# Kernel tuning notes

Measured on AMD Instinct MI355X. Metric: run time of the kernel, lower is better.

## Reference

```python
import jax, jax.numpy as jnp
import numpy as np

N, NFEAT, NHID, NCLASS, ATT = 4096, 512, 128, 16, 64


def _glorot(key, shape):
    lim = 1.0 / np.sqrt(shape[0])
    return jax.random.uniform(key, shape, jnp.float32, -lim, lim)


def setup_inputs() -> dict:
    key = jax.random.key(0)
    ks = jax.random.split(key, 26)
    inp = {
        "A0": jax.random.uniform(ks[0], (N, N), jnp.float32),
        "A1": jax.random.uniform(ks[1], (N, N), jnp.float32),
        "A2": jax.random.uniform(ks[2], (N, N), jnp.float32),
        "x": jax.random.normal(ks[3], (N, NFEAT), jnp.float32),
        # attention-over-adjacency projections: Linear(N, ATT)
        "Wa1": _glorot(ks[4], (N, ATT)), "ba1": jnp.zeros((ATT,), jnp.float32),
        "Wa2": _glorot(ks[5], (N, ATT)), "ba2": jnp.zeros((ATT,), jnp.float32),
        "Wa3": _glorot(ks[6], (N, ATT)), "ba3": jnp.zeros((ATT,), jnp.float32),
        # agg: Linear(3*ATT, 3)
        "Wagg": _glorot(ks[7], (3 * ATT, 3)), "bagg": jnp.zeros((3,), jnp.float32),
        # gcn1: nfeat -> nhid
        "W1": _glorot(ks[8], (NFEAT, NHID)), "b1": jnp.zeros((NHID,), jnp.float32),
        # Q/K/V: nhid -> nhid
        "Wq": _glorot(ks[9], (NHID, NHID)), "bq": jnp.zeros((NHID,), jnp.float32),
        "Wk": _glorot(ks[10], (NHID, NHID)), "bk": jnp.zeros((NHID,), jnp.float32),
        "Wv": _glorot(ks[11], (NHID, NHID)), "bv": jnp.zeros((NHID,), jnp.float32),
        # gcn2: nhid -> nclass
        "W2": _glorot(ks[12], (NHID, NCLASS)), "b2": jnp.zeros((NCLASS,), jnp.float32),
    }
    return inp


def _gcn_norm(a):
    # symmetric degree normalization D^-1/2 A D^-1/2 (zero-safe)
    d = a.sum(axis=1)
    dinv = jnp.where(d > 0, jax.lax.rsqrt(jnp.maximum(d, 1e-12)), 0.0)
    return dinv[:, None] * a * dinv[None, :]


def reference(A0, A1, A2, x, Wa1, ba1, Wa2, ba2, Wa3, ba3, Wagg, bagg,
              W1, b1, Wq, bq, Wk, bk, Wv, bv, W2, b2):
    # per-adjacency attention logits over rows -> mixing weights per node
    z1 = A0 @ Wa1 + ba1                      # [N, ATT]
    z2 = A1 @ Wa2 + ba2
    z3 = A2 @ Wa3 + ba3
    z4 = jnp.concatenate([z1, z2, z3], axis=1) @ Wagg + bagg   # [N, 3]
    nz = jax.nn.softmax(z4, axis=1)
    # torch broadcasting: nz[:, k] (shape [N]) scales COLUMNS of [N,N]
    adj = (A0 * nz[:, 0][None, :] + A1 * nz[:, 1][None, :]
           + A2 * nz[:, 2][None, :])                           # [N, N]
    # gcn1 + relu
    h = jax.nn.relu(adj @ (x @ W1) + b1)                       # [N, NHID]
    Qh = h @ Wq + bq
    Kh = h @ Wk + bk
    Vh = h @ Wv + bv
    # adjacency-masked QK^T, row softmax, degree norm, mix with V
    A_tilde = adj * (Qh @ Kh.T)                                # [N, N]
    attention = jax.nn.softmax(A_tilde, axis=1)
    X_tilde = jax.nn.relu(_gcn_norm(attention) @ Vh)           # [N, NHID]
    # gcn2
    z = adj @ (X_tilde @ W2) + b2                              # [N, NCLASS]
    return jax.nn.softmax(z, axis=1), nz
```

## Files before the change

### kernel.cpp

```cpp
#include <hip/hip_runtime.h>
#include <math.h>

#define N 4096
#define NF 512
#define NH 128
#define NC 16
#define CSPLIT 8

typedef unsigned short u16;
typedef __attribute__((ext_vector_type(4))) unsigned short u16x4;
typedef __attribute__((ext_vector_type(8))) short bf16x8;
typedef __attribute__((ext_vector_type(4))) float f32x4;

__device__ __forceinline__ u16 hi16(float v) {
  return (u16)(__float_as_uint(v) >> 16);
}
__device__ __forceinline__ float hif(float v) {
  return __uint_as_float(__float_as_uint(v) & 0xffff0000u);
}

__global__ void k_wc(const float* __restrict__ Wa1, const float* __restrict__ Wa2,
                     const float* __restrict__ Wa3, const float* __restrict__ Wagg,
                     const float* __restrict__ ba1, const float* __restrict__ ba2,
                     const float* __restrict__ ba3, const float* __restrict__ bagg,
                     float* __restrict__ Wc2, float* __restrict__ bz) {
  int idx = blockIdx.x * 256 + threadIdx.x;
  if (idx < 3 * N) {
    int k = idx >> 12;
    int j = idx & (N - 1);
    const float* Wa = (k == 0) ? Wa1 : (k == 1) ? Wa2 : Wa3;
    float a0 = 0.f, a1 = 0.f, a2 = 0.f;
    for (int t = 0; t < 64; ++t) {
      float w = Wa[j * 64 + t];
      const float* wg = Wagg + (k * 64 + t) * 3;
      a0 += w * wg[0]; a1 += w * wg[1]; a2 += w * wg[2];
    }
    float4 o = {a0, a1, a2, 0.f};
    *(float4*)&Wc2[(k * N + j) * 4] = o;
  }
  if (blockIdx.x == 0 && threadIdx.x < 3) {
    int c = threadIdx.x;
    float acc = bagg[c];
    for (int t = 0; t < 64; ++t) {
      acc += ba1[t] * Wagg[t * 3 + c]
           + ba2[t] * Wagg[(64 + t) * 3 + c]
           + ba3[t] * Wagg[(128 + t) * 3 + c];
    }
    bz[c] = acc;
  }
}

__global__ __launch_bounds__(256) void k_z4p(const float* __restrict__ A,
                                             const float* __restrict__ Wck,
                                             float* __restrict__ zpk) {
  __shared__ float red[4][3][4];
  int r0 = blockIdx.x * 4;
  int tid = threadIdx.x;
  int lane = tid & 63, wv = tid >> 6;
  float acc[4][3];
#pragma unroll
  for (int r = 0; r < 4; ++r) { acc[r][0] = 0.f; acc[r][1] = 0.f; acc[r][2] = 0.f; }
#pragma unroll
  for (int s = 0; s < 4; ++s) {
    int j4 = s * 1024 + tid * 4;
    const float4 w0 = *(const float4*)&Wck[(j4 + 0) * 4];
    const float4 w1 = *(const float4*)&Wck[(j4 + 1) * 4];
    const float4 w2 = *(const float4*)&Wck[(j4 + 2) * 4];
    const float4 w3 = *(const float4*)&Wck[(j4 + 3) * 4];
#pragma unroll
    for (int r = 0; r < 4; ++r) {
      const float4 a = *(const float4*)&A[(size_t)(r0 + r) * N + j4];
      acc[r][0] += a.x * w0.x + a.y * w1.x + a.z * w2.x + a.w * w3.x;
      acc[r][1] += a.x * w0.y + a.y * w1.y + a.z * w2.y + a.w * w3.y;
      acc[r][2] += a.x * w0.z + a.y * w1.z + a.z * w2.z + a.w * w3.z;
    }
  }
#pragma unroll
  for (int r = 0; r < 4; ++r) {
#pragma unroll
    for (int c = 0; c < 3; ++c) {
      float v = acc[r][c];
      v += __shfl_xor(v, 1);
      v += __shfl_xor(v, 2);
      v += __shfl_xor(v, 4);
      v += __shfl_xor(v, 8);
      v += __shfl_xor(v, 16);
      v += __shfl_xor(v, 32);
      if (lane == 0) red[r][c][wv] = v;
    }
  }
  __syncthreads();
  if (tid < 12) {
    int r = tid / 3; int c = tid - 3 * r;
    zpk[(r0 + r) * 12 + c] =
        red[r][c][0] + red[r][c][1] + red[r][c][2] + red[r][c][3];
  }
}

__global__ void k_nz(const float* __restrict__ zp, const float* __restrict__ bz,
                     float* __restrict__ nz) {
  int row = blockIdx.x * 256 + threadIdx.x;
  const float* p = zp + row * 12;
  float z0 = p[0] + p[3] + p[6] + bz[0];
  float z1 = p[1] + p[4] + p[7] + bz[1];
  float z2 = p[2] + p[5] + p[8] + bz[2];
  float m = fmaxf(z0, fmaxf(z1, z2));
  float e0 = __expf(z0 - m), e1 = __expf(z1 - m), e2 = __expf(z2 - m);
  float s = e0 + e1 + e2;
  float* o = nz + row * 3;
  o[0] = e0 / s; o[1] = e1 / s; o[2] = e2 / s;
}

__global__ void k_adj(const float* __restrict__ A0, const float* __restrict__ A1,
                      const float* __restrict__ A2, const float* __restrict__ nz,
                      float* __restrict__ adj) {
  int idx = blockIdx.x * 256 + threadIdx.x;
  int i = idx >> 10;
  int j4 = (idx & 1023) << 2;
  int base = i * N + j4;
  const float4 a0 = *(const float4*)&A0[base];
  const float4 a1 = *(const float4*)&A1[base];
  const float4 a2 = *(const float4*)&A2[base];
  const float4 n0 = *(const float4*)&nz[j4 * 3];
  const float4 n1 = *(const float4*)&nz[j4 * 3 + 4];
  const float4 n2 = *(const float4*)&nz[j4 * 3 + 8];
  float4 o;
  o.x = a0.x * n0.x + a1.x * n0.y + a2.x * n0.z;
  o.y = a0.y * n0.w + a1.y * n1.x + a2.y * n1.y;
  o.z = a0.z * n1.z + a1.z * n1.w + a2.z * n2.x;
  o.w = a0.w * n2.y + a1.w * n2.z + a2.w * n2.w;
  *(float4*)&adj[base] = o;
}

__global__ void k_wsplit(const float* __restrict__ Wq, const float* __restrict__ Wk,
                         const float* __restrict__ Wv, const float* __restrict__ W1,
                         u16* __restrict__ WThi, u16* __restrict__ WTlo,
                         u16* __restrict__ W1Thi, u16* __restrict__ W1Tlo) {
  int idx = blockIdx.x * 256 + threadIdx.x;
  if (idx < 49152) {
    int gm = idx >> 14;
    int rem = idx & 16383;
    int col = rem >> 7, k = rem & 127;
    const float* W = (gm == 0) ? Wq : (gm == 1) ? Wk : Wv;
    float v = W[k * NH + col];
    WThi[idx] = hi16(v);
    WTlo[idx] = hi16(v - hif(v));
  } else {
    int rem = idx - 49152;
    int col = rem >> 9, k = rem & 511;
    float v = W1[k * NH + col];
    W1Thi[rem] = hi16(v);
    W1Tlo[rem] = hi16(v - hif(v));
  }
}

__global__ __launch_bounds__(256) void k_xw1m(
    const float* __restrict__ x,
    const u16* __restrict__ W1Thi, const u16* __restrict__ W1Tlo,
    u16* __restrict__ xw1Thi, u16* __restrict__ xw1Tlo) {
  __shared__ u16 Ah[64][128];
  __shared__ u16 Al[64][128];
  __shared__ u16 Vst[2][128 * 24];
  int i0 = blockIdx.x * 16;
  int tid = threadIdx.x;
  int w = tid >> 6, l = tid & 63, g = l >> 4, l15 = l & 15;
  {
    int r = tid >> 4, cb = (tid & 15) * 4;
#pragma unroll
    for (int q = 0; q < 4; ++q) {
      int c = cb + q;
      const float4 a0 = *(const float4*)&x[(size_t)(i0 + r) * NF + c * 8];
      const float4 a1 = *(const float4*)&x[(size_t)(i0 + r) * NF + c * 8 + 4];
      bf16x8 hi8, lo8;
      const float* p0 = (const float*)&a0;
      const float* p1 = (const float*)&a1;
#pragma unroll
      for (int e = 0; e < 4; ++e) {
        float v0 = p0[e], v1 = p1[e];
        hi8[e] = (short)hi16(v0); hi8[4 + e] = (short)hi16(v1);
        lo8[e] = (short)hi16(v0 - hif(v0));
        lo8[4 + e] = (short)hi16(v1 - hif(v1));
      }
      *(bf16x8*)&Ah[c][r * 8] = hi8;
      *(bf16x8*)&Al[c][r * 8] = lo8;
    }
  }
  __syncthreads();
  f32x4 acc[2];
  acc[0] = (f32x4){0.f, 0.f, 0.f, 0.f};
  acc[1] = (f32x4){0.f, 0.f, 0.f, 0.f};
#pragma unroll 4
  for (int kb = 0; kb < 16; ++kb) {
    const bf16x8 ah = *(const bf16x8*)&Ah[kb * 4 + g][l15 * 8];
    const bf16x8 al = *(const bf16x8*)&Al[kb * 4 + g][l15 * 8];
#pragma unroll
    for (int cti = 0; cti < 2; ++cti) {
      int col = (2 * w + cti) * 16 + l15;
      const bf16x8 bh = *(const bf16x8*)&W1Thi[col * NF + kb * 32 + 8 * g];
      const bf16x8 bl = *(const bf16x8*)&W1Tlo[col * NF + kb * 32 + 8 * g];
      acc[cti] = __builtin_amdgcn_mfma_f32_16x16x32_bf16(ah, bh, acc[cti], 0, 0, 0);
      acc[cti] = __builtin_amdgcn_mfma_f32_16x16x32_bf16(ah, bl, acc[cti], 0, 0, 0);
      acc[cti] = __builtin_amdgcn_mfma_f32_16x16x32_bf16(al, bh, acc[cti], 0, 0, 0);
    }
  }
#pragma unroll
  for (int cti = 0; cti < 2; ++cti) {
    int col = (2 * w + cti) * 16 + l15;
#pragma unroll
    for (int i = 0; i < 4; ++i) {
      float v = acc[cti][i];
      Vst[0][col * 24 + 4 * g + i] = hi16(v);
      Vst[1][col * 24 + 4 * g + i] = hi16(v - hif(v));
    }
  }
  __syncthreads();
  {
    int d = tid >> 1, half = tid & 1;
    bf16x8 vh = *(const bf16x8*)&Vst[0][d * 24 + half * 8];
    bf16x8 vl = *(const bf16x8*)&Vst[1][d * 24 + half * 8];
    *(bf16x8*)&xw1Thi[(size_t)d * N + i0 + half * 8] = vh;
    *(bf16x8*)&xw1Tlo[(size_t)d * N + i0 + half * 8] = vl;
  }
}

__device__ __forceinline__ void glds16(const void* g, void* l) {
  __builtin_amdgcn_global_load_lds(
      (const __attribute__((address_space(1))) void*)g,
      (__attribute__((address_space(3))) void*)l, 16, 0, 0);
}

__global__ __launch_bounds__(512) void k_h(const float* __restrict__ adj,
                                           const u16* __restrict__ xw1Thi,
                                           const u16* __restrict__ xw1Tlo,
                                           float* __restrict__ hp0,
                                           float* __restrict__ hp1,
                                           float* __restrict__ hp2,
                                           float* __restrict__ hp3) {
  __shared__ u16 Ah[8][512];
  __shared__ u16 Al[8][512];
  __shared__ u16 Bh[8][1024];
  __shared__ u16 Bl[8][1024];
  int i0 = blockIdx.x * 64;
  int kbase = blockIdx.y * 1024;
  float* hp = (blockIdx.y == 0) ? hp0 : (blockIdx.y == 1) ? hp1
            : (blockIdx.y == 2) ? hp2 : hp3;
  int tid = threadIdx.x;
  int w = tid >> 6, l = tid & 63, g = l >> 4, l15 = l & 15;
  int rt = w & 3, cg = w >> 2;
  int srow = tid >> 3, sseg = tid & 7;

  f32x4 acc[4];
#pragma unroll
  for (int nt = 0; nt < 4; ++nt) acc[nt] = (f32x4){0.f, 0.f, 0.f, 0.f};

  for (int t = 0; t < 16; ++t) {
    int k0 = kbase + t * 64;
    const float4 av0 = *(const float4*)&adj[(size_t)(i0 + srow) * N + k0 + sseg * 8];
    const float4 av1 = *(const float4*)&adj[(size_t)(i0 + srow) * N + k0 + sseg * 8 + 4];
    asm volatile("s_waitcnt lgkmcnt(0)" ::: "memory");
    __builtin_amdgcn_s_barrier();
#pragma unroll
    for (int q = 0; q < 4; ++q) {
      int idx = w * 4 + q;
      int buf = idx >> 4, kk = (idx >> 1) & 7, hf = idx & 1;
      const u16* src = buf ? xw1Tlo : xw1Thi;
      u16* dst = buf ? &Bl[kk][hf * 512] : &Bh[kk][hf * 512];
      glds16(&src[(size_t)(hf * 64 + l) * N + k0 + kk * 8], dst);
    }
    asm volatile("s_waitcnt vmcnt(4)" ::: "memory");
    {
      bf16x8 hi8, lo8;
      const float* a0p = (const float*)&av0;
      const float* a1p = (const float*)&av1;
#pragma unroll
      for (int e = 0; e < 4; ++e) {
        float v0 = a0p[e], v1 = a1p[e];
        hi8[e] = (short)hi16(v0);     hi8[4 + e] = (short)hi16(v1);
        lo8[e] = (short)hi16(v0 - hif(v0));
        lo8[4 + e] = (short)hi16(v1 - hif(v1));
      }
      *(bf16x8*)&Ah[sseg][srow * 8] = hi8;
      *(bf16x8*)&Al[sseg][srow * 8] = lo8;
    }
    asm volatile("s_waitcnt vmcnt(0) lgkmcnt(0)" ::: "memory");
    __builtin_amdgcn_s_barrier();

#pragma unroll
    for (int kb = 0; kb < 2; ++kb) {
      const bf16x8 ah = *(const bf16x8*)&Ah[kb * 4 + g][(rt * 16 + l15) * 8];
      const bf16x8 al = *(const bf16x8*)&Al[kb * 4 + g][(rt * 16 + l15) * 8];
#pragma unroll
      for (int nt = 0; nt < 4; ++nt) {
        int col = cg * 64 + nt * 16 + l15;
        const bf16x8 bh = *(const bf16x8*)&Bh[kb * 4 + g][col * 8];
        const bf16x8 bl = *(const bf16x8*)&Bl[kb * 4 + g][col * 8];
        acc[nt] = __builtin_amdgcn_mfma_f32_16x16x32_bf16(ah, bh, acc[nt], 0, 0, 0);
        acc[nt] = __builtin_amdgcn_mfma_f32_16x16x32_bf16(ah, bl, acc[nt], 0, 0, 0);
        acc[nt] = __builtin_amdgcn_mfma_f32_16x16x32_bf16(al, bh, acc[nt], 0, 0, 0);
      }
    }
  }
#pragma unroll
  for (int nt = 0; nt < 4; ++nt)
#pragma unroll
    for (int i = 0; i < 4; ++i)
      hp[(size_t)(i0 + rt * 16 + 4 * g + i) * NH + cg * 64 + nt * 16 + l15] =
          acc[nt][i];
}

__global__ void k_hsum(const float* __restrict__ hp0, const float* __restrict__ hp1,
                       const float* __restrict__ hp2, const float* __restrict__ hp3,
                       const float* __restrict__ b1,
                       u16* __restrict__ Hhi, u16* __restrict__ Hlo) {
  int idx = blockIdx.x * 256 + threadIdx.x;
  int gi = idx * 4;
  const float4 v0 = *(const float4*)&hp0[gi];
  const float4 v1 = *(const float4*)&hp1[gi];
  const float4 v2 = *(const float4*)&hp2[gi];
  const float4 v3 = *(const float4*)&hp3[gi];
  const float4 bv = *(const float4*)&b1[gi & (NH - 1)];
  float h[4];
  h[0] = fmaxf(v0.x + v1.x + v2.x + v3.x + bv.x, 0.f);
  h[1] = fmaxf(v0.y + v1.y + v2.y + v3.y + bv.y, 0.f);
  h[2] = fmaxf(v0.z + v1.z + v2.z + v3.z + bv.z, 0.f);
  h[3] = fmaxf(v0.w + v1.w + v2.w + v3.w + bv.w, 0.f);
  u16x4 hi, lo;
#pragma unroll
  for (int e = 0; e < 4; ++e) {
    hi[e] = hi16(h[e]);
    lo[e] = hi16(h[e] - hif(h[e]));
  }
  *(u16x4*)&Hhi[gi] = hi;
  *(u16x4*)&Hlo[gi] = lo;
}

__global__ __launch_bounds__(256) void k_qkv2(
    const u16* __restrict__ Hhi, const u16* __restrict__ Hlo,
    const u16* __restrict__ WThi, const u16* __restrict__ WTlo,
    const float* __restrict__ bq, const float* __restrict__ bk,
    const float* __restrict__ bv,
    u16* __restrict__ Qhi, u16* __restrict__ Qlo,
    u16* __restrict__ Khi, u16* __restrict__ Klo,
    u16* __restrict__ VThi, u16* __restrict__ VTlo) {
  __shared__ u16 Vst[2][128 * 24];
  int i0 = blockIdx.x * 16;
  int tid = threadIdx.x;
  int w = tid >> 6, l = tid & 63, g = l >> 4, l15 = l & 15;
  bf16x8 ah[4], al[4];
#pragma unroll
  for (int kb = 0; kb < 4; ++kb) {
    ah[kb] = *(const bf16x8*)&Hhi[(i0 + l15) * NH + kb * 32 + 8 * g];
    al[kb] = *(const bf16x8*)&Hlo[(i0 + l15) * NH + kb * 32 + 8 * g];
  }
#pragma unroll
  for (int gm = 0; gm < 3; ++gm) {
    const u16* wth = WThi + gm * 16384;
    const u16* wtl = WTlo + gm * 16384;
    const float* bb = (gm == 0) ? bq : (gm == 1) ? bk : bv;
#pragma unroll
    for (int cti = 0; cti < 2; ++cti) {
      int ct = 2 * w + cti;
      int col = ct * 16 + l15;
      f32x4 acc = (f32x4){0.f, 0.f, 0.f, 0.f};
#pragma unroll
      for (int kb = 0; kb < 4; ++kb) {
        const bf16x8 bh = *(const bf16x8*)&wth[col * NH + kb * 32 + 8 * g];
        const bf16x8 bl = *(const bf16x8*)&wtl[col * NH + kb * 32 + 8 * g];
        acc = __builtin_amdgcn_mfma_f32_16x16x32_bf16(ah[kb], bh, acc, 0, 0, 0);
        acc = __builtin_amdgcn_mfma_f32_16x16x32_bf16(ah[kb], bl, acc, 0, 0, 0);
        acc = __builtin_amdgcn_mfma_f32_16x16x32_bf16(al[kb], bh, acc, 0, 0, 0);
      }
      float bias = bb[col];
#pragma unroll
      for (int i = 0; i < 4; ++i) {
        float v = acc[i] + bias;
        u16 vh = hi16(v), vl = hi16(v - hif(v));
        int row = i0 + 4 * g + i;
        if (gm == 0) {
          Qhi[row * NH + col] = vh; Qlo[row * NH + col] = vl;
        } else if (gm == 1) {
          Khi[row * NH + col] = vh; Klo[row * NH + col] = vl;
        } else {
          Vst[0][col * 24 + 4 * g + i] = vh;
          Vst[1][col * 24 + 4 * g + i] = vl;
        }
      }
    }
  }
  __syncthreads();
  {
    int d = tid >> 1, half = tid & 1;
    bf16x8 vh = *(const bf16x8*)&Vst[0][d * 24 + half * 8];
    bf16x8 vl = *(const bf16x8*)&Vst[1][d * 24 + half * 8];
    *(bf16x8*)&VThi[(size_t)d * N + i0 + half * 8] = vh;
    *(bf16x8*)&VTlo[(size_t)d * N + i0 + half * 8] = vl;
  }
}

__global__ __launch_bounds__(512) void k_attn(
    const u16* __restrict__ Qhi, const u16* __restrict__ Qlo,
    const u16* __restrict__ Khi, const u16* __restrict__ Klo,
    const u16* __restrict__ VThi, const u16* __restrict__ VTlo,
    const float* __restrict__ adj,
    float* __restrict__ xp0, float* __restrict__ xp1, float* __restrict__ xp2,
    float* __restrict__ xp3, float* __restrict__ xp4, float* __restrict__ xp5,
    float* __restrict__ xp6, float* __restrict__ xp7,
    float* __restrict__ ml) {
  __shared__ u16 Ks[2][16][512];
  __shared__ u16 Vs[2][8][1024];
  __shared__ u16 Ps[2][8][1024];
  int i0 = blockIdx.x * 128;
  int cid = blockIdx.y;
  int tid = threadIdx.x;
  int w = tid >> 6, l = tid & 63, g = l >> 4, l15 = l & 15;
  int ty = tid >> 4, tx16 = tid & 15;
  float* xp = (cid < 4) ? ((cid < 2) ? (cid == 0 ? xp0 : xp1) : (cid == 2 ? xp2 : xp3))
                        : ((cid < 6) ? (cid == 4 ? xp4 : xp5) : (cid == 6 ? xp6 : xp7));

  bf16x8 qh[4], ql[4];
  {
    const u16* qbh = &Qhi[(i0 + 16 * w + l15) * NH];
    const u16* qbl = &Qlo[(i0 + 16 * w + l15) * NH];
#pragma unroll
    for (int kb = 0; kb < 4; ++kb) {
      qh[kb] = *(const bf16x8*)&qbh[kb * 32 + 8 * g];
      ql[kb] = *(const bf16x8*)&qbl[kb * 32 + 8 * g];
    }
  }

  float m[4], li[4];
  f32x4 Xa[8];
#pragma unroll
  for (int i = 0; i < 4; ++i) { m[i] = -3.0e38f; li[i] = 0.f; }
#pragma unroll
  for (int nt = 0; nt < 8; ++nt) Xa[nt] = (f32x4){0.f, 0.f, 0.f, 0.f};

  for (int jt = 0; jt < 8; ++jt) {
    int j0g = cid * (N / CSPLIT) + jt * 64;
    float adjm[4][4];
#pragma unroll
    for (int i = 0; i < 4; ++i)
#pragma unroll
      for (int ct = 0; ct < 4; ++ct)
        adjm[i][ct] = adj[(i0 + 4 * ty + i) * N + j0g + ct * 16 + tx16];
    asm volatile("s_waitcnt lgkmcnt(0)" ::: "memory");
    __builtin_amdgcn_s_barrier();
#pragma unroll
    for (int q = 0; q < 4; ++q) {
      int idx = w * 4 + q;
      int buf = idx >> 4, c = idx & 15;
      const u16* ks = buf ? Klo : Khi;
      glds16(&ks[(j0g + l) * NH + c * 8], &Ks[buf][c][0]);
    }
#pragma unroll
    for (int q = 0; q < 4; ++q) {
      int idx = w * 4 + q;
      int buf = idx >> 4, cj = (idx >> 1) & 7, h = idx & 1;
      const u16* vsrc = buf ? VTlo : VThi;
      glds16(&vsrc[(h * 64 + l) * N + j0g + cj * 8], &Vs[buf][cj][h * 512]);
    }
    asm volatile("s_waitcnt vmcnt(4)" ::: "memory");
    __builtin_amdgcn_s_barrier();

    f32x4 acc[4];
#pragma unroll
    for (int ct = 0; ct < 4; ++ct) acc[ct] = (f32x4){0.f, 0.f, 0.f, 0.f};
#pragma unroll
    for (int kb = 0; kb < 4; ++kb) {
#pragma unroll
      for (int ct = 0; ct < 4; ++ct) {
        const bf16x8 kh = *(const bf16x8*)&Ks[0][kb * 4 + g][(ct * 16 + l15) * 8];
        const bf16x8 kl = *(const bf16x8*)&Ks[1][kb * 4 + g][(ct * 16 + l15) * 8];
        acc[ct] = __builtin_amdgcn_mfma_f32_16x16x32_bf16(qh[kb], kh, acc[ct], 0, 0, 0);
        acc[ct] = __builtin_amdgcn_mfma_f32_16x16x32_bf16(qh[kb], kl, acc[ct], 0, 0, 0);
        acc[ct] = __builtin_amdgcn_mfma_f32_16x16x32_bf16(ql[kb], kh, acc[ct], 0, 0, 0);
      }
    }

#pragma unroll
    for (int i = 0; i < 4; ++i) {
      float p[4];
      float s0 = acc[0][i] * adjm[i][0];
      float s1 = acc[1][i] * adjm[i][1];
      float s2 = acc[2][i] * adjm[i][2];
      float s3 = acc[3][i] * adjm[i][3];
      float t = fmaxf(fmaxf(s0, s1), fmaxf(s2, s3));
      t = fmaxf(t, __shfl_xor(t, 1));
      t = fmaxf(t, __shfl_xor(t, 2));
      t = fmaxf(t, __shfl_xor(t, 4));
      t = fmaxf(t, __shfl_xor(t, 8));
      float mn = fmaxf(m[i], t);
      float sc = __expf(m[i] - mn);
      p[0] = __expf(s0 - mn); p[1] = __expf(s1 - mn);
      p[2] = __expf(s2 - mn); p[3] = __expf(s3 - mn);
      float ps = p[0] + p[1] + p[2] + p[3];
      ps += __shfl_xor(ps, 1);
      ps += __shfl_xor(ps, 2);
      ps += __shfl_xor(ps, 4);
      ps += __shfl_xor(ps, 8);
      li[i] = li[i] * sc + ps;
      m[i] = mn;
#pragma unroll
      for (int nt = 0; nt < 8; ++nt) Xa[nt][i] *= sc;
      int row = 4 * ty + i;
#pragma unroll
      for (int ct = 0; ct < 4; ++ct) {
        float pe = p[ct];
        float po = __shfl_xor(pe, 1);
        int cj = ct * 2 + (tx16 >> 3);
        int e = (ct * 16 + tx16) & 7;
        unsigned int hpk = (__float_as_uint(po) & 0xffff0000u)
                         | (__float_as_uint(pe) >> 16);
        float pel = pe - hif(pe), pol = po - hif(po);
        unsigned int lpk = (__float_as_uint(pol) & 0xffff0000u)
                         | (__float_as_uint(pel) >> 16);
        if (!(tx16 & 1)) {
          *(unsigned int*)&Ps[0][cj][row * 8 + e] = hpk;
          *(unsigned int*)&Ps[1][cj][row * 8 + e] = lpk;
        }
      }
    }
    asm volatile("s_waitcnt vmcnt(0)" ::: "memory");
    __builtin_amdgcn_s_barrier();

#pragma unroll
    for (int jb = 0; jb < 2; ++jb) {
      const bf16x8 ph = *(const bf16x8*)&Ps[0][jb * 4 + g][(16 * w + l15) * 8];
      const bf16x8 pl = *(const bf16x8*)&Ps[1][jb * 4 + g][(16 * w + l15) * 8];
#pragma unroll
      for (int nt = 0; nt < 8; ++nt) {
        const bf16x8 vh = *(const bf16x8*)&Vs[0][jb * 4 + g][(nt * 16 + l15) * 8];
        const bf16x8 vl = *(const bf16x8*)&Vs[1][jb * 4 + g][(nt * 16 + l15) * 8];
        Xa[nt] = __builtin_amdgcn_mfma_f32_16x16x32_bf16(ph, vh, Xa[nt], 0, 0, 0);
        Xa[nt] = __builtin_amdgcn_mfma_f32_16x16x32_bf16(ph, vl, Xa[nt], 0, 0, 0);
        Xa[nt] = __builtin_amdgcn_mfma_f32_16x16x32_bf16(pl, vh, Xa[nt], 0, 0, 0);
      }
    }
  }

#pragma unroll
  for (int i = 0; i < 4; ++i) {
    int row = i0 + 4 * ty + i;
    float inv = 1.f / li[i];
#pragma unroll
    for (int nt = 0; nt < 8; ++nt)
      xp[row * NH + nt * 16 + tx16] = Xa[nt][i] * inv;
    if (tx16 == 0) {
      ml[(cid * N + row) * 2 + 0] = m[i];
      ml[(cid * N + row) * 2 + 1] = li[i];
    }
  }
}

__global__ void k_comb(const float* __restrict__ xp0, const float* __restrict__ xp1,
                       const float* __restrict__ xp2, const float* __restrict__ xp3,
                       const float* __restrict__ xp4, const float* __restrict__ xp5,
                       const float* __restrict__ xp6, const float* __restrict__ xp7,
                       const float* __restrict__ ml, float* __restrict__ Xt) {
  int idx = blockIdx.x * 256 + threadIdx.x;
  int r = idx >> 5, d4 = (idx & 31) << 2;
  float mm[8], ll[8];
#pragma unroll
  for (int c = 0; c < 8; ++c) {
    mm[c] = ml[(c * N + r) * 2 + 0];
    ll[c] = ml[(c * N + r) * 2 + 1];
  }
  float ms = mm[0];
#pragma unroll
  for (int c = 1; c < 8; ++c) ms = fmaxf(ms, mm[c]);
  float e[8], den = 0.f;
#pragma unroll
  for (int c = 0; c < 8; ++c) { e[c] = __expf(mm[c] - ms); den += e[c] * ll[c]; }
  float inv = 1.f / den;
  const float4 a0 = *(const float4*)&xp0[r * NH + d4];
  const float4 a1 = *(const float4*)&xp1[r * NH + d4];
  const float4 a2 = *(const float4*)&xp2[r * NH + d4];
  const float4 a3 = *(const float4*)&xp3[r * NH + d4];
  const float4 a4 = *(const float4*)&xp4[r * NH + d4];
  const float4 a5 = *(const float4*)&xp5[r * NH + d4];
  const float4 a6 = *(const float4*)&xp6[r * NH + d4];
  const float4 a7 = *(const float4*)&xp7[r * NH + d4];
  float4 o;
  o.x = a0.x * e[0] + a1.x * e[1] + a2.x * e[2] + a3.x * e[3]
      + a4.x * e[4] + a5.x * e[5] + a6.x * e[6] + a7.x * e[7];
  o.y = a0.y * e[0] + a1.y * e[1] + a2.y * e[2] + a3.y * e[3]
      + a4.y * e[4] + a5.y * e[5] + a6.y * e[6] + a7.y * e[7];
  o.z = a0.z * e[0] + a1.z * e[1] + a2.z * e[2] + a3.z * e[3]
      + a4.z * e[4] + a5.z * e[5] + a6.z * e[6] + a7.z * e[7];
  o.w = a0.w * e[0] + a1.w * e[1] + a2.w * e[2] + a3.w * e[3]
      + a4.w * e[4] + a5.w * e[5] + a6.w * e[6] + a7.w * e[7];
  o.x = fmaxf(o.x * inv, 0.f); o.y = fmaxf(o.y * inv, 0.f);
  o.z = fmaxf(o.z * inv, 0.f); o.w = fmaxf(o.w * inv, 0.f);
  *(float4*)&Xt[r * NH + d4] = o;
}

__global__ __launch_bounds__(256) void k_xtw2(const float* __restrict__ Xt,
                                              const float* __restrict__ W2,
                                              float* __restrict__ xtw2) {
  __shared__ float xs[16 * 132];
  __shared__ float w2s[NH * NC];
  int i0 = blockIdx.x * 16;
  int tid = threadIdx.x;
#pragma unroll
  for (int s = 0; s < 2; ++s) {
    int f4 = tid + 256 * s;
    int r = f4 >> 5, k4 = (f4 & 31) << 2;
    const float4 v = *(const float4*)&Xt[(i0 + r) * NH + k4];
    *(float4*)&xs[r * 132 + k4] = v;
    *(float4*)&w2s[f4 * 4] = *(const float4*)&W2[f4 * 4];
  }
  __syncthreads();
  int r = tid >> 4, c = tid & 15;
  float acc = 0.f;
#pragma unroll 8
  for (int k = 0; k < NH; ++k)
    acc += xs[r * 132 + k] * w2s[k * NC + c];
  xtw2[(i0 + r) * NC + c] = acc;
}

__global__ __launch_bounds__(256) void k_z(const float* __restrict__ adj,
                                           const float* __restrict__ xtw2,
                                           const float* __restrict__ b2,
                                           float* __restrict__ out) {
  __shared__ float xwsT[16 * 68];
  int i0 = blockIdx.x * 8;
  int tid = threadIdx.x;
  int ty = tid >> 6, cg = (tid >> 4) & 3, jg = tid & 15;
  int jr = tid >> 2, cq = tid & 3;
  float acc[2][4];
#pragma unroll
  for (int i = 0; i < 2; ++i)
#pragma unroll
    for (int c = 0; c < 4; ++c) acc[i][c] = 0.f;

  for (int j0 = 0; j0 < N; j0 += 64) {
    float4 av[2];
#pragma unroll
    for (int i = 0; i < 2; ++i)
      av[i] = *(const float4*)&adj[(i0 + 2 * ty + i) * N + j0 + 4 * jg];
    const float4 xv = *(const float4*)&xtw2[(j0 + jr) * NC + 4 * cq];
    __syncthreads();
    xwsT[(4 * cq + 0) * 68 + jr] = xv.x;
    xwsT[(4 * cq + 1) * 68 + jr] = xv.y;
    xwsT[(4 * cq + 2) * 68 + jr] = xv.z;
    xwsT[(4 * cq + 3) * 68 + jr] = xv.w;
    __syncthreads();
#pragma unroll
    for (int c = 0; c < 4; ++c) {
      const float4 wv = *(const float4*)&xwsT[(4 * cg + c) * 68 + 4 * jg];
#pragma unroll
      for (int i = 0; i < 2; ++i)
        acc[i][c] += av[i].x * wv.x + av[i].y * wv.y
                   + av[i].z * wv.z + av[i].w * wv.w;
    }
  }
#pragma unroll
  for (int i = 0; i < 2; ++i)
#pragma unroll
    for (int c = 0; c < 4; ++c) {
      float v = acc[i][c];
      v += __shfl_xor(v, 1);
      v += __shfl_xor(v, 2);
      v += __shfl_xor(v, 4);
      v += __shfl_xor(v, 8);
      acc[i][c] = v;
    }
  float bv0 = b2[4 * cg + 0], bv1 = b2[4 * cg + 1];
  float bv2 = b2[4 * cg + 2], bv3 = b2[4 * cg + 3];
#pragma unroll
  for (int i = 0; i < 2; ++i) {
    float z0 = acc[i][0] + bv0, z1 = acc[i][1] + bv1;
    float z2 = acc[i][2] + bv2, z3 = acc[i][3] + bv3;
    float mv = fmaxf(fmaxf(z0, z1), fmaxf(z2, z3));
    mv = fmaxf(mv, __shfl_xor(mv, 16));
    mv = fmaxf(mv, __shfl_xor(mv, 32));
    float e0 = __expf(z0 - mv), e1 = __expf(z1 - mv);
    float e2 = __expf(z2 - mv), e3 = __expf(z3 - mv);
    float s = e0 + e1 + e2 + e3;
    s += __shfl_xor(s, 16);
    s += __shfl_xor(s, 32);
    if (jg == 0) {
      float4 o = {e0 / s, e1 / s, e2 / s, e3 / s};
      *(float4*)&out[(i0 + 2 * ty + i) * NC + 4 * cg] = o;
    }
  }
}

extern "C" void kernel_launch(void* const* d_in, const int* in_sizes, int n_in,
                              void* d_out, int out_size, void* d_ws, size_t ws_size,
                              hipStream_t stream) {
  const float* A0  = (const float*)d_in[0];
  const float* A1  = (const float*)d_in[1];
  const float* A2  = (const float*)d_in[2];
  const float* x   = (const float*)d_in[3];
  const float* Wa1 = (const float*)d_in[4];  const float* ba1 = (const float*)d_in[5];
  const float* Wa2 = (const float*)d_in[6];  const float* ba2 = (const float*)d_in[7];
  const float* Wa3 = (const float*)d_in[8];  const float* ba3 = (const float*)d_in[9];
  const float* Wagg = (const float*)d_in[10]; const float* bagg = (const float*)d_in[11];
  const float* W1  = (const float*)d_in[12]; const float* b1  = (const float*)d_in[13];
  const float* Wq  = (const float*)d_in[14]; const float* bq  = (const float*)d_in[15];
  const float* Wk  = (const float*)d_in[16]; const float* bk  = (const float*)d_in[17];
  const float* Wv  = (const float*)d_in[18]; const float* bv  = (const float*)d_in[19];
  const float* W2  = (const float*)d_in[20]; const float* b2  = (const float*)d_in[21];

  float* out0 = (float*)d_out;
  float* nz   = out0 + N * NC;

  float* ws   = (float*)d_ws;
  float* adj  = ws;
  float* Wc2  = adj + (size_t)N * N;
  float* bz   = Wc2 + 3 * N * 4;
  float* xw1  = bz + 16;
  float* hpre = xw1 + N * NH;
  float* QhT  = hpre + N * NH;
  float* KhT  = QhT + N * NH;
  float* Vh   = KhT + N * NH;
  float* Xt   = Vh + N * NH;
  float* xtw2 = Xt + N * NH;
  float* P2   = xtw2 + N * NC;
  float* P3   = P2 + N * NH;
  float* P4   = P3 + N * NH;
  float* P5   = P4 + N * NH;
  float* P6   = P5 + N * NH;
  float* ml   = P6 + N * NH;
  float* zp   = QhT;

  u16* xw1Thi = (u16*)xw1; u16* xw1Tlo = xw1Thi + (size_t)N * NH;
  u16* Qhi  = (u16*)QhT; u16* Qlo = Qhi + (size_t)N * NH;
  u16* Khi  = (u16*)KhT; u16* Klo = Khi + (size_t)N * NH;
  u16* VThi = (u16*)Vh;  u16* VTlo = VThi + (size_t)N * NH;
  u16* Hhi  = (u16*)Xt;  u16* Hlo = Hhi + (size_t)N * NH;
  u16* WThi = (u16*)xtw2; u16* WTlo = WThi + (size_t)3 * NH * NH;
  u16* W1Thi = (u16*)(QhT + 65536); u16* W1Tlo = W1Thi + (size_t)NF * NH;

  hipLaunchKernelGGL(k_wc, dim3(48), dim3(256), 0, stream,
                     Wa1, Wa2, Wa3, Wagg, ba1, ba2, ba3, bagg, Wc2, bz);
  hipLaunchKernelGGL(k_wsplit, dim3(448), dim3(256), 0, stream,
                     Wq, Wk, Wv, W1, WThi, WTlo, W1Thi, W1Tlo);
  hipLaunchKernelGGL(k_z4p, dim3(N / 4), dim3(256), 0, stream,
                     A0, Wc2 + 0 * N * 4, zp + 0);
  hipLaunchKernelGGL(k_z4p, dim3(N / 4), dim3(256), 0, stream,
                     A1, Wc2 + 1 * N * 4, zp + 3);
  hipLaunchKernelGGL(k_z4p, dim3(N / 4), dim3(256), 0, stream,
                     A2, Wc2 + 2 * N * 4, zp + 6);
  hipLaunchKernelGGL(k_nz, dim3(N / 256), dim3(256), 0, stream, zp, bz, nz);
  hipLaunchKernelGGL(k_adj, dim3(N * N / 4 / 256), dim3(256), 0, stream,
                     A0, A1, A2, nz, adj);
  hipLaunchKernelGGL(k_xw1m, dim3(N / 16), dim3(256), 0, stream,
                     x, W1Thi, W1Tlo, xw1Thi, xw1Tlo);
  hipLaunchKernelGGL(k_h, dim3(N / 64, 4), dim3(512), 0, stream,
                     adj, xw1Thi, xw1Tlo, hpre, P2, P3, P4);
  hipLaunchKernelGGL(k_hsum, dim3(N * NH / 4 / 256), dim3(256), 0, stream,
                     hpre, P2, P3, P4, b1, Hhi, Hlo);
  hipLaunchKernelGGL(k_qkv2, dim3(N / 16), dim3(256), 0, stream,
                     Hhi, Hlo, WThi, WTlo, bq, bk, bv,
                     Qhi, Qlo, Khi, Klo, VThi, VTlo);
  hipLaunchKernelGGL(k_attn, dim3(N / 128, CSPLIT), dim3(512), 0, stream,
                     Qhi, Qlo, Khi, Klo, VThi, VTlo, adj,
                     xw1, hpre, P2, P3, P4, P5, P6, Xt, ml);
  hipLaunchKernelGGL(k_comb, dim3(N * NH / 4 / 256), dim3(256), 0, stream,
                     xw1, hpre, P2, P3, P4, P5, P6, Xt, ml, Xt);
  hipLaunchKernelGGL(k_xtw2, dim3(N / 16), dim3(256), 0, stream, Xt, W2, xtw2);
  hipLaunchKernelGGL(k_z, dim3(N / 8), dim3(256), 0, stream, adj, xtw2, b2, out0);
}
```

Before: 292.6 us.

## Register-prefetch k_h tiles, swizzle B LDS layout, reorder grid axes

In k_h, the direct global-to-LDS loads are replaced by register prefetching of the next k-tile of adj and xw1T while the current tile is computed. The B tile in LDS gets an XOR swizzle and the A tile gets padding, both to reduce bank conflicts. The grid dimensions of k_h and k_attn are swapped so that blocks sharing the same row tile (different k or column splits) launch next to each other, which may improve L2 reuse. The cost is higher register pressure from the prefetch buffers.

```diff
diff --git a/kernel.cpp b/kernel.cpp
--- a/kernel.cpp
+++ b/kernel.cpp
@@ -17,6 +17,9 @@
 }
 __device__ __forceinline__ float hif(float v) {
   return __uint_as_float(__float_as_uint(v) & 0xffff0000u);
+}
+__device__ __forceinline__ int idxB(int col) {
+  return (col * 8) ^ (col & 0x38);
 }
 
 __global__ void k_wc(const float* __restrict__ Wa1, const float* __restrict__ Wa2,
@@ -236,38 +239,42 @@
                                            float* __restrict__ hp1,
                                            float* __restrict__ hp2,
                                            float* __restrict__ hp3) {
-  __shared__ u16 Ah[8][512];
-  __shared__ u16 Al[8][512];
+  __shared__ u16 Ah[8][520];
+  __shared__ u16 Al[8][520];
   __shared__ u16 Bh[8][1024];
   __shared__ u16 Bl[8][1024];
-  int i0 = blockIdx.x * 64;
-  int kbase = blockIdx.y * 1024;
-  float* hp = (blockIdx.y == 0) ? hp0 : (blockIdx.y == 1) ? hp1
-            : (blockIdx.y == 2) ? hp2 : hp3;
+  int kbase = blockIdx.x * 1024;
+  int i0 = blockIdx.y * 64;
+  float* hp = (blockIdx.x == 0) ? hp0 : (blockIdx.x == 1) ? hp1
+            : (blockIdx.x == 2) ? hp2 : hp3;
   int tid = threadIdx.x;
   int w = tid >> 6, l = tid & 63, g = l >> 4, l15 = l & 15;
   int rt = w & 3, cg = w >> 2;
   int srow = tid >> 3, sseg = tid & 7;
+  int bkk[4], bbuf[4], bcol[4];
+#pragma unroll
+  for (int q = 0; q < 4; ++q) {
+    int idx = w * 4 + q;
+    bbuf[q] = idx >> 4; bkk[q] = (idx >> 1) & 7;
+    bcol[q] = (idx & 1) * 64 + l;
+  }
+
+  float4 av0 = *(const float4*)&adj[(size_t)(i0 + srow) * N + kbase + sseg * 8];
+  float4 av1 = *(const float4*)&adj[(size_t)(i0 + srow) * N + kbase + sseg * 8 + 4];
+  bf16x8 breg[4];
+#pragma unroll
+  for (int q = 0; q < 4; ++q) {
+    const u16* src = bbuf[q] ? xw1Tlo : xw1Thi;
+    breg[q] = *(const bf16x8*)&src[(size_t)bcol[q] * N + kbase + bkk[q] * 8];
+  }
 
   f32x4 acc[4];
 #pragma unroll
   for (int nt = 0; nt < 4; ++nt) acc[nt] = (f32x4){0.f, 0.f, 0.f, 0.f};
 
   for (int t = 0; t < 16; ++t) {
-    int k0 = kbase + t * 64;
-    const float4 av0 = *(const float4*)&adj[(size_t)(i0 + srow) * N + k0 + sseg * 8];
-    const float4 av1 = *(const float4*)&adj[(size_t)(i0 + srow) * N + k0 + sseg * 8 + 4];
     asm volatile("s_waitcnt lgkmcnt(0)" ::: "memory");
     __builtin_amdgcn_s_barrier();
-#pragma unroll
-    for (int q = 0; q < 4; ++q) {
-      int idx = w * 4 + q;
-      int buf = idx >> 4, kk = (idx >> 1) & 7, hf = idx & 1;
-      const u16* src = buf ? xw1Tlo : xw1Thi;
-      u16* dst = buf ? &Bl[kk][hf * 512] : &Bh[kk][hf * 512];
-      glds16(&src[(size_t)(hf * 64 + l) * N + k0 + kk * 8], dst);
-    }
-    asm volatile("s_waitcnt vmcnt(4)" ::: "memory");
     {
       bf16x8 hi8, lo8;
       const float* a0p = (const float*)&av0;
@@ -282,7 +289,22 @@
       *(bf16x8*)&Ah[sseg][srow * 8] = hi8;
       *(bf16x8*)&Al[sseg][srow * 8] = lo8;
     }
-    asm volatile("s_waitcnt vmcnt(0) lgkmcnt(0)" ::: "memory");
+#pragma unroll
+    for (int q = 0; q < 4; ++q) {
+      u16* dst = bbuf[q] ? &Bl[bkk[q]][0] : &Bh[bkk[q]][0];
+      *(bf16x8*)&dst[idxB(bcol[q])] = breg[q];
+    }
+    if (t < 15) {
+      int k0n = kbase + (t + 1) * 64;
+      av0 = *(const float4*)&adj[(size_t)(i0 + srow) * N + k0n + sseg * 8];
+      av1 = *(const float4*)&adj[(size_t)(i0 + srow) * N + k0n + sseg * 8 + 4];
+#pragma unroll
+      for (int q = 0; q < 4; ++q) {
+        const u16* src = bbuf[q] ? xw1Tlo : xw1Thi;
+        breg[q] = *(const bf16x8*)&src[(size_t)bcol[q] * N + k0n + bkk[q] * 8];
+      }
+    }
+    asm volatile("s_waitcnt lgkmcnt(0)" ::: "memory");
     __builtin_amdgcn_s_barrier();
 
 #pragma unroll
@@ -292,8 +314,8 @@
 #pragma unroll
       for (int nt = 0; nt < 4; ++nt) {
         int col = cg * 64 + nt * 16 + l15;
-        const bf16x8 bh = *(const bf16x8*)&Bh[kb * 4 + g][col * 8];
-        const bf16x8 bl = *(const bf16x8*)&Bl[kb * 4 + g][col * 8];
+        const bf16x8 bh = *(const bf16x8*)&Bh[kb * 4 + g][idxB(col)];
+        const bf16x8 bl = *(const bf16x8*)&Bl[kb * 4 + g][idxB(col)];
         acc[nt] = __builtin_amdgcn_mfma_f32_16x16x32_bf16(ah, bh, acc[nt], 0, 0, 0);
         acc[nt] = __builtin_amdgcn_mfma_f32_16x16x32_bf16(ah, bl, acc[nt], 0, 0, 0);
         acc[nt] = __builtin_amdgcn_mfma_f32_16x16x32_bf16(al, bh, acc[nt], 0, 0, 0);
@@ -409,8 +431,8 @@
   __shared__ u16 Ks[2][16][512];
   __shared__ u16 Vs[2][8][1024];
   __shared__ u16 Ps[2][8][1024];
-  int i0 = blockIdx.x * 128;
-  int cid = blockIdx.y;
+  int cid = blockIdx.x;
+  int i0 = blockIdx.y * 128;
   int tid = threadIdx.x;
   int w = tid >> 6, l = tid & 63, g = l >> 4, l15 = l & 15;
   int ty = tid >> 4, tx16 = tid & 15;
@@ -748,14 +770,14 @@
                      A0, A1, A2, nz, adj);
   hipLaunchKernelGGL(k_xw1m, dim3(N / 16), dim3(256), 0, stream,
                      x, W1Thi, W1Tlo, xw1Thi, xw1Tlo);
-  hipLaunchKernelGGL(k_h, dim3(N / 64, 4), dim3(512), 0, stream,
+  hipLaunchKernelGGL(k_h, dim3(4, N / 64), dim3(512), 0, stream,
                      adj, xw1Thi, xw1Tlo, hpre, P2, P3, P4);
   hipLaunchKernelGGL(k_hsum, dim3(N * NH / 4 / 256), dim3(256), 0, stream,
                      hpre, P2, P3, P4, b1, Hhi, Hlo);
   hipLaunchKernelGGL(k_qkv2, dim3(N / 16), dim3(256), 0, stream,
                      Hhi, Hlo, WThi, WTlo, bq, bk, bv,
                      Qhi, Qlo, Khi, Klo, VThi, VTlo);
-  hipLaunchKernelGGL(k_attn, dim3(N / 128, CSPLIT), dim3(512), 0, stream,
+  hipLaunchKernelGGL(k_attn, dim3(CSPLIT, N / 128), dim3(512), 0, stream,
                      Qhi, Qlo, Khi, Klo, VThi, VTlo, adj,
                      xw1, hpre, P2, P3, P4, P5, P6, Xt, ml);
   hipLaunchKernelGGL(k_comb, dim3(N * NH / 4 / 256), dim3(256), 0, stream,
```

After: 270.2 us. 1.08x faster.
